# Optimization experiments

Measured on AMD Instinct MI355X. Metric: run time of the kernel, lower is better.

Reference implementation:

```python
import jax, jax.numpy as jnp
import numpy as np

N = 131072
K = 1024
D = 64

def setup_inputs() -> dict:
    key = jax.random.key(0)
    k1, k2 = jax.random.split(key)
    x = jax.random.normal(k1, (N, D), dtype=jnp.float32)
    emb_weight = jax.random.normal(k2, (K, D), dtype=jnp.float32)
    return {"x": x, "emb_weight": emb_weight}

def reference(x, emb_weight):
    distances = (
        jnp.sum(x * x, axis=1, keepdims=True)
        + jnp.sum(emb_weight * emb_weight, axis=1)
        - 2.0 * jnp.matmul(x, emb_weight.T)
    )
    codebook_indices = jnp.argmin(distances, axis=1)  # [N]
    probs = jax.nn.one_hot(codebook_indices, K, dtype=x.dtype)  # [N, K]
    z_q = emb_weight[codebook_indices]  # [N, D]
    return (z_q, probs)
```

## Files before the change

kernel.cpp:

```cpp
#include <hip/hip_runtime.h>
#include <math.h>

#define N_TOK 131072
#define K_CB  1024
#define D_DIM 64
#define MARGIN 0.0625f

#define WS_EN     0
#define WS_ES     4096
#define WS_CNT    266240
#define WS_LIST   266248

#define FILL_BLOCKS 2048
#define PREP_BLOCKS 16

typedef short bf16x8 __attribute__((ext_vector_type(8)));
typedef float f32x4  __attribute__((ext_vector_type(4)));

__device__ __forceinline__ ushort f2bf(float f) {
    uint u = __float_as_uint(f);
    u += 0x7FFFu + ((u >> 16) & 1u);
    return (ushort)(u >> 16);
}
__device__ __forceinline__ float bf2f(ushort h) {
    return __uint_as_float(((uint)h) << 16);
}

__global__ __launch_bounds__(256) void fill_and_prep(
    float* __restrict__ probs, const float* __restrict__ emb,
    float* __restrict__ en, ushort* __restrict__ es, uint* __restrict__ fixcnt)
{
    const int tid = threadIdx.x;
    const int blk = blockIdx.x;
    if (blk < FILL_BLOCKS) {
        f32x4* p = (f32x4*)probs + (size_t)blk * 16384 + tid;
        const f32x4 zero4 = {0.f, 0.f, 0.f, 0.f};
        #pragma unroll
        for (int i = 0; i < 64; ++i) p[i * 256] = zero4;
        return;
    }
    const int pb   = blk - FILL_BLOCKS;
    const int c6   = tid & 63;
    const int q    = tid >> 6;
    const int code = pb * 64 + c6;
    if (pb == 0 && tid == 0) *fixcnt = 0;

    const float* er = emb + (size_t)code * D_DIM;
    #pragma unroll
    for (int j = 0; j < 16; ++j) {
        float f = er[q * 16 + j];
        ushort h = f2bf(f);
        es[(size_t)code * 128 + q * 16 + j]      = h;
        es[(size_t)code * 128 + 64 + q * 16 + j] = f2bf(f - bf2f(h));
    }
    if (q == 0) {
        float s = 0.f;
        #pragma unroll
        for (int d = 0; d < D_DIM; ++d) s = fmaf(er[d], er[d], s);
        en[code] = s;
    }
}

__global__ __launch_bounds__(256) void vq_main(
    const float* __restrict__ x, const float* __restrict__ emb,
    const float* __restrict__ en, const ushort* __restrict__ es,
    float* __restrict__ zq, float* __restrict__ probs,
    uint* __restrict__ fixcnt, uint* __restrict__ fixlist, uint fixcap)
{
    const int tid  = threadIdx.x;
    const int wave = tid >> 6, lane = tid & 63;
    const int quad = lane >> 4, l15 = lane & 15;
    const int blockRow = blockIdx.x * 128;
    const int waveRow  = blockRow + wave * 32;

    __shared__ uint  lds_k[128];
    __shared__ float lds_en[K_CB];

    {
        f32x4 v = ((const f32x4*)en)[tid];
        ((f32x4*)lds_en)[tid] = v;
    }

    bf16x8 af[2][4];
    #pragma unroll
    for (int g = 0; g < 2; ++g) {
        const float* xr = x + (size_t)(waveRow + g * 16 + l15) * D_DIM + quad * 8;
        f32x4 p0 = *(const f32x4*)(xr);
        f32x4 p1 = *(const f32x4*)(xr + 4);
        f32x4 p2 = *(const f32x4*)(xr + 32);
        f32x4 p3 = *(const f32x4*)(xr + 36);
        float v0[8], v1[8];
        #pragma unroll
        for (int j = 0; j < 4; ++j) { v0[j] = p0[j]; v0[4 + j] = p1[j]; v1[j] = p2[j]; v1[4 + j] = p3[j]; }
        #pragma unroll
        for (int j = 0; j < 8; ++j) {
            ushort h0 = f2bf(v0[j]);
            af[g][0][j] = (short)h0;
            af[g][2][j] = (short)f2bf(v0[j] - bf2f(h0));
            ushort h1 = f2bf(v1[j]);
            af[g][1][j] = (short)h1;
            af[g][3][j] = (short)f2bf(v1[j] - bf2f(h1));
        }
    }
    __syncthreads();

    float b1[8], b2[8]; int k1[8];
    #pragma unroll
    for (int s = 0; s < 8; ++s) { b1[s] = INFINITY; b2[s] = INFINITY; k1[s] = 0; }

    const bf16x8* __restrict__ esv = (const bf16x8*)es;

    for (int cb = 0; cb < 64; ++cb) {
        const int code = cb * 16 + l15;
        bf16x8 bfr[4];
        #pragma unroll
        for (int ks = 0; ks < 4; ++ks) bfr[ks] = esv[(size_t)code * 16 + ks * 4 + quad];

        f32x4 acc0 = {0.f, 0.f, 0.f, 0.f};
        f32x4 acc1 = {0.f, 0.f, 0.f, 0.f};
        acc0 = __builtin_amdgcn_mfma_f32_16x16x32_bf16(af[0][0], bfr[0], acc0, 0, 0, 0);
        acc0 = __builtin_amdgcn_mfma_f32_16x16x32_bf16(af[0][1], bfr[1], acc0, 0, 0, 0);
        acc0 = __builtin_amdgcn_mfma_f32_16x16x32_bf16(af[0][0], bfr[2], acc0, 0, 0, 0);
        acc0 = __builtin_amdgcn_mfma_f32_16x16x32_bf16(af[0][1], bfr[3], acc0, 0, 0, 0);
        acc0 = __builtin_amdgcn_mfma_f32_16x16x32_bf16(af[0][2], bfr[0], acc0, 0, 0, 0);
        acc0 = __builtin_amdgcn_mfma_f32_16x16x32_bf16(af[0][3], bfr[1], acc0, 0, 0, 0);
        acc1 = __builtin_amdgcn_mfma_f32_16x16x32_bf16(af[1][0], bfr[0], acc1, 0, 0, 0);
        acc1 = __builtin_amdgcn_mfma_f32_16x16x32_bf16(af[1][1], bfr[1], acc1, 0, 0, 0);
        acc1 = __builtin_amdgcn_mfma_f32_16x16x32_bf16(af[1][0], bfr[2], acc1, 0, 0, 0);
        acc1 = __builtin_amdgcn_mfma_f32_16x16x32_bf16(af[1][1], bfr[3], acc1, 0, 0, 0);
        acc1 = __builtin_amdgcn_mfma_f32_16x16x32_bf16(af[1][2], bfr[0], acc1, 0, 0, 0);
        acc1 = __builtin_amdgcn_mfma_f32_16x16x32_bf16(af[1][3], bfr[1], acc1, 0, 0, 0);

        const float env = lds_en[code];
        #pragma unroll
        for (int r = 0; r < 4; ++r) {
            {
                float d = fmaf(-2.f, acc0[r], env);
                bool lt = d < b1[r];
                b2[r] = lt ? b1[r] : fminf(b2[r], d);
                k1[r] = lt ? code : k1[r];
                b1[r] = lt ? d : b1[r];
            }
            {
                int s = 4 + r;
                float d = fmaf(-2.f, acc1[r], env);
                bool lt = d < b1[s];
                b2[s] = lt ? b1[s] : fminf(b2[s], d);
                k1[s] = lt ? code : k1[s];
                b1[s] = lt ? d : b1[s];
            }
        }
    }

    #pragma unroll
    for (int s = 0; s < 8; ++s) {
        #pragma unroll
        for (int off = 1; off < 16; off <<= 1) {
            float ob1 = __shfl_xor(b1[s], off);
            int   ok1 = __shfl_xor(k1[s], off);
            float ob2 = __shfl_xor(b2[s], off);
            bool better = (ob1 < b1[s]) || (ob1 == b1[s] && ok1 < k1[s]);
            float loser = better ? b1[s] : ob1;
            b1[s] = better ? ob1 : b1[s];
            k1[s] = better ? ok1 : k1[s];
            b2[s] = fminf(fminf(b2[s], ob2), loser);
        }
    }
    if (l15 == 0) {
        #pragma unroll
        for (int s = 0; s < 8; ++s) {
            int g = s >> 2, r = s & 3;
            int lrow = wave * 32 + g * 16 + quad * 4 + r;
            uint word = (uint)k1[s];
            if (b2[s] - b1[s] <= MARGIN) word |= 0x80000000u;
            lds_k[lrow] = word;
        }
    }
    __syncthreads();

    if (tid < 128) {
        uint w = lds_k[tid];
        uint kk = w & 0x3FFu;
        probs[(size_t)(blockRow + tid) * K_CB + kk] = 1.0f;
        if (w & 0x80000000u) {
            uint idx = atomicAdd(fixcnt, 1u);
            if (idx < fixcap) fixlist[idx] = (uint)(blockRow + tid) | (kk << 17);
        }
    }

    #pragma unroll
    for (int t = 0; t < 8; ++t) {
        int i = tid + t * 256;
        int r = i >> 4, c = i & 15;
        int kk = (int)(lds_k[r] & 0x3FFu);
        f32x4 v = ((const f32x4*)(emb + (size_t)kk * D_DIM))[c];
        ((f32x4*)(zq + (size_t)(blockRow + r) * D_DIM))[c] = v;
    }
}

__global__ __launch_bounds__(256) void vq_fixup(
    const float* __restrict__ x, const float* __restrict__ emb,
    const float* __restrict__ en,
    float* __restrict__ zq, float* __restrict__ probs,
    const uint* __restrict__ fixcnt, const uint* __restrict__ fixlist, uint fixcap)
{
    const int lane = threadIdx.x & 63;
    const uint gwave = (uint)((blockIdx.x * 256 + threadIdx.x) >> 6);
    uint cnt = *fixcnt;
    if (cnt > fixcap) cnt = fixcap;

    for (uint e = gwave; e < cnt; e += 1024u) {
        uint w = fixlist[e];
        int row = (int)(w & 0x1FFFFu);
        int kg  = (int)(w >> 17);
        const float* xr = x + (size_t)row * D_DIM;
        float xn = 0.f;
        #pragma unroll
        for (int d = 0; d < D_DIM; ++d) xn = fmaf(xr[d], xr[d], xn);

        float bd = INFINITY; int bk = 0;
        for (int t = 0; t < 16; ++t) {
            int code = t * 64 + lane;
            const float* er = emb + (size_t)code * D_DIM;
            float a0 = 0.f, a1 = 0.f, a2 = 0.f, a3 = 0.f;
            #pragma unroll
            for (int d = 0; d < D_DIM; d += 4) {
                a0 = fmaf(xr[d + 0], er[d + 0], a0);
                a1 = fmaf(xr[d + 1], er[d + 1], a1);
                a2 = fmaf(xr[d + 2], er[d + 2], a2);
                a3 = fmaf(xr[d + 3], er[d + 3], a3);
            }
            float acc = (a0 + a1) + (a2 + a3);
            float dist = fmaf(-2.f, acc, xn + en[code]);
            if (dist < bd) { bd = dist; bk = code; }
        }
        #pragma unroll
        for (int off = 1; off < 64; off <<= 1) {
            float od = __shfl_xor(bd, off);
            int   ok = __shfl_xor(bk, off);
            if (od < bd || (od == bd && ok < bk)) { bd = od; bk = ok; }
        }
        if (bk != kg) {
            if (lane == 0) {
                probs[(size_t)row * K_CB + kg] = 0.f;
                probs[(size_t)row * K_CB + bk] = 1.f;
            }
            if (lane < 16)
                ((f32x4*)(zq + (size_t)row * D_DIM))[lane] =
                    ((const f32x4*)(emb + (size_t)bk * D_DIM))[lane];
        }
    }
}

extern "C" void kernel_launch(void* const* d_in, const int* in_sizes, int n_in,
                              void* d_out, int out_size, void* d_ws, size_t ws_size,
                              hipStream_t stream) {
    const float* x   = (const float*)d_in[0];
    const float* emb = (const float*)d_in[1];
    float* zq    = (float*)d_out;
    float* probs = (float*)d_out + (size_t)N_TOK * D_DIM;

    char* ws = (char*)d_ws;
    float*  en      = (float*)(ws + WS_EN);
    ushort* es      = (ushort*)(ws + WS_ES);
    uint*   fixcnt  = (uint*)(ws + WS_CNT);
    uint*   fixlist = (uint*)(ws + WS_LIST);
    uint fixcap = (ws_size > WS_LIST + 4) ? (uint)((ws_size - WS_LIST) / 4) : 0u;

    fill_and_prep<<<FILL_BLOCKS + PREP_BLOCKS, 256, 0, stream>>>(probs, emb, en, es, fixcnt);
    vq_main<<<N_TOK / 128, 256, 0, stream>>>(x, emb, en, es, zq, probs, fixcnt, fixlist, fixcap);
    vq_fixup<<<256, 256, 0, stream>>>(x, emb, en, zq, probs, fixcnt, fixlist, fixcap);
}
```

Before: 773.0 us.

## Fuse one-hot probs write into main kernel and halve rows per block

Removes the separate zero-fill pass over the 512MB probs tensor. The main kernel now writes each full one-hot row itself with nontemporal vector stores, so probs is written once instead of being zeroed and then scattered into. Each block now handles 64 rows, one 16-row MFMA group per wave. The LDS copy of the code norms and the block barriers are gone, and norms are read from global memory instead. The trade-off is that the matmul phase now carries the heavy store traffic inline, and each wave gets half the codebook reuse per load.

```diff
diff --git a/kernel.cpp b/kernel.cpp
--- a/kernel.cpp
+++ b/kernel.cpp
@@ -11,9 +11,6 @@
 #define WS_CNT    266240
 #define WS_LIST   266248
 
-#define FILL_BLOCKS 2048
-#define PREP_BLOCKS 16
-
 typedef short bf16x8 __attribute__((ext_vector_type(8)));
 typedef float f32x4  __attribute__((ext_vector_type(4)));
 
@@ -26,22 +23,14 @@
     return __uint_as_float(((uint)h) << 16);
 }
 
-__global__ __launch_bounds__(256) void fill_and_prep(
-    float* __restrict__ probs, const float* __restrict__ emb,
-    float* __restrict__ en, ushort* __restrict__ es, uint* __restrict__ fixcnt)
+__global__ __launch_bounds__(256) void prep_kernel(
+    const float* __restrict__ emb, float* __restrict__ en,
+    ushort* __restrict__ es, uint* __restrict__ fixcnt)
 {
     const int tid = threadIdx.x;
-    const int blk = blockIdx.x;
-    if (blk < FILL_BLOCKS) {
-        f32x4* p = (f32x4*)probs + (size_t)blk * 16384 + tid;
-        const f32x4 zero4 = {0.f, 0.f, 0.f, 0.f};
-        #pragma unroll
-        for (int i = 0; i < 64; ++i) p[i * 256] = zero4;
-        return;
-    }
-    const int pb   = blk - FILL_BLOCKS;
-    const int c6   = tid & 63;
-    const int q    = tid >> 6;
+    const int pb  = blockIdx.x;
+    const int c6  = tid & 63;
+    const int q   = tid >> 6;
     const int code = pb * 64 + c6;
     if (pb == 0 && tid == 0) *fixcnt = 0;
 
@@ -61,7 +50,7 @@
     }
 }
 
-__global__ __launch_bounds__(256) void vq_main(
+__global__ __launch_bounds__(256) void vq_onehot(
     const float* __restrict__ x, const float* __restrict__ emb,
     const float* __restrict__ en, const ushort* __restrict__ es,
     float* __restrict__ zq, float* __restrict__ probs,
@@ -70,21 +59,11 @@
     const int tid  = threadIdx.x;
     const int wave = tid >> 6, lane = tid & 63;
     const int quad = lane >> 4, l15 = lane & 15;
-    const int blockRow = blockIdx.x * 128;
-    const int waveRow  = blockRow + wave * 32;
-
-    __shared__ uint  lds_k[128];
-    __shared__ float lds_en[K_CB];
-
+    const int waveRow = blockIdx.x * 64 + wave * 16;
+
+    bf16x8 af[4];
     {
-        f32x4 v = ((const f32x4*)en)[tid];
-        ((f32x4*)lds_en)[tid] = v;
-    }
-
-    bf16x8 af[2][4];
-    #pragma unroll
-    for (int g = 0; g < 2; ++g) {
-        const float* xr = x + (size_t)(waveRow + g * 16 + l15) * D_DIM + quad * 8;
+        const float* xr = x + (size_t)(waveRow + l15) * D_DIM + quad * 8;
         f32x4 p0 = *(const f32x4*)(xr);
         f32x4 p1 = *(const f32x4*)(xr + 4);
         f32x4 p2 = *(const f32x4*)(xr + 32);
@@ -95,18 +74,17 @@
         #pragma unroll
         for (int j = 0; j < 8; ++j) {
             ushort h0 = f2bf(v0[j]);
-            af[g][0][j] = (short)h0;
-            af[g][2][j] = (short)f2bf(v0[j] - bf2f(h0));
+            af[0][j] = (short)h0;
+            af[2][j] = (short)f2bf(v0[j] - bf2f(h0));
             ushort h1 = f2bf(v1[j]);
-            af[g][1][j] = (short)h1;
-            af[g][3][j] = (short)f2bf(v1[j] - bf2f(h1));
-        }
-    }
-    __syncthreads();
-
-    float b1[8], b2[8]; int k1[8];
-    #pragma unroll
-    for (int s = 0; s < 8; ++s) { b1[s] = INFINITY; b2[s] = INFINITY; k1[s] = 0; }
+            af[1][j] = (short)h1;
+            af[3][j] = (short)f2bf(v1[j] - bf2f(h1));
+        }
+    }
+
+    float b1[4], b2[4]; int k1[4];
+    #pragma unroll
+    for (int r = 0; r < 4; ++r) { b1[r] = INFINITY; b2[r] = INFINITY; k1[r] = 0; }
 
     const bf16x8* __restrict__ esv = (const bf16x8*)es;
 
@@ -116,85 +94,66 @@
         #pragma unroll
         for (int ks = 0; ks < 4; ++ks) bfr[ks] = esv[(size_t)code * 16 + ks * 4 + quad];
 
-        f32x4 acc0 = {0.f, 0.f, 0.f, 0.f};
-        f32x4 acc1 = {0.f, 0.f, 0.f, 0.f};
-        acc0 = __builtin_amdgcn_mfma_f32_16x16x32_bf16(af[0][0], bfr[0], acc0, 0, 0, 0);
-        acc0 = __builtin_amdgcn_mfma_f32_16x16x32_bf16(af[0][1], bfr[1], acc0, 0, 0, 0);
-        acc0 = __builtin_amdgcn_mfma_f32_16x16x32_bf16(af[0][0], bfr[2], acc0, 0, 0, 0);
-        acc0 = __builtin_amdgcn_mfma_f32_16x16x32_bf16(af[0][1], bfr[3], acc0, 0, 0, 0);
-        acc0 = __builtin_amdgcn_mfma_f32_16x16x32_bf16(af[0][2], bfr[0], acc0, 0, 0, 0);
-        acc0 = __builtin_amdgcn_mfma_f32_16x16x32_bf16(af[0][3], bfr[1], acc0, 0, 0, 0);
-        acc1 = __builtin_amdgcn_mfma_f32_16x16x32_bf16(af[1][0], bfr[0], acc1, 0, 0, 0);
-        acc1 = __builtin_amdgcn_mfma_f32_16x16x32_bf16(af[1][1], bfr[1], acc1, 0, 0, 0);
-        acc1 = __builtin_amdgcn_mfma_f32_16x16x32_bf16(af[1][0], bfr[2], acc1, 0, 0, 0);
-        acc1 = __builtin_amdgcn_mfma_f32_16x16x32_bf16(af[1][1], bfr[3], acc1, 0, 0, 0);
-        acc1 = __builtin_amdgcn_mfma_f32_16x16x32_bf16(af[1][2], bfr[0], acc1, 0, 0, 0);
-        acc1 = __builtin_amdgcn_mfma_f32_16x16x32_bf16(af[1][3], bfr[1], acc1, 0, 0, 0);
-
-        const float env = lds_en[code];
+        f32x4 acc = {0.f, 0.f, 0.f, 0.f};
+        acc = __builtin_amdgcn_mfma_f32_16x16x32_bf16(af[0], bfr[0], acc, 0, 0, 0);
+        acc = __builtin_amdgcn_mfma_f32_16x16x32_bf16(af[1], bfr[1], acc, 0, 0, 0);
+        acc = __builtin_amdgcn_mfma_f32_16x16x32_bf16(af[0], bfr[2], acc, 0, 0, 0);
+        acc = __builtin_amdgcn_mfma_f32_16x16x32_bf16(af[1], bfr[3], acc, 0, 0, 0);
+        acc = __builtin_amdgcn_mfma_f32_16x16x32_bf16(af[2], bfr[0], acc, 0, 0, 0);
+        acc = __builtin_amdgcn_mfma_f32_16x16x32_bf16(af[3], bfr[1], acc, 0, 0, 0);
+
+        const float env = en[code];
         #pragma unroll
         for (int r = 0; r < 4; ++r) {
-            {
-                float d = fmaf(-2.f, acc0[r], env);
-                bool lt = d < b1[r];
-                b2[r] = lt ? b1[r] : fminf(b2[r], d);
-                k1[r] = lt ? code : k1[r];
-                b1[r] = lt ? d : b1[r];
-            }
-            {
-                int s = 4 + r;
-                float d = fmaf(-2.f, acc1[r], env);
-                bool lt = d < b1[s];
-                b2[s] = lt ? b1[s] : fminf(b2[s], d);
-                k1[s] = lt ? code : k1[s];
-                b1[s] = lt ? d : b1[s];
-            }
-        }
-    }
-
-    #pragma unroll
-    for (int s = 0; s < 8; ++s) {
+            float d = fmaf(-2.f, acc[r], env);
+            bool lt = d < b1[r];
+            b2[r] = lt ? b1[r] : fminf(b2[r], d);
+            k1[r] = lt ? code : k1[r];
+            b1[r] = lt ? d : b1[r];
+        }
+    }
+
+    #pragma unroll
+    for (int r = 0; r < 4; ++r) {
         #pragma unroll
         for (int off = 1; off < 16; off <<= 1) {
-            float ob1 = __shfl_xor(b1[s], off);
-            int   ok1 = __shfl_xor(k1[s], off);
-            float ob2 = __shfl_xor(b2[s], off);
-            bool better = (ob1 < b1[s]) || (ob1 == b1[s] && ok1 < k1[s]);
-            float loser = better ? b1[s] : ob1;
-            b1[s] = better ? ob1 : b1[s];
-            k1[s] = better ? ok1 : k1[s];
-            b2[s] = fminf(fminf(b2[s], ob2), loser);
-        }
-    }
-    if (l15 == 0) {
-        #pragma unroll
-        for (int s = 0; s < 8; ++s) {
-            int g = s >> 2, r = s & 3;
-            int lrow = wave * 32 + g * 16 + quad * 4 + r;
-            uint word = (uint)k1[s];
-            if (b2[s] - b1[s] <= MARGIN) word |= 0x80000000u;
-            lds_k[lrow] = word;
-        }
-    }
-    __syncthreads();
-
-    if (tid < 128) {
-        uint w = lds_k[tid];
-        uint kk = w & 0x3FFu;
-        probs[(size_t)(blockRow + tid) * K_CB + kk] = 1.0f;
-        if (w & 0x80000000u) {
+            float ob1 = __shfl_xor(b1[r], off);
+            int   ok1 = __shfl_xor(k1[r], off);
+            float ob2 = __shfl_xor(b2[r], off);
+            bool better = (ob1 < b1[r]) || (ob1 == b1[r] && ok1 < k1[r]);
+            float loser = better ? b1[r] : ob1;
+            b1[r] = better ? ob1 : b1[r];
+            k1[r] = better ? ok1 : k1[r];
+            b2[r] = fminf(fminf(b2[r], ob2), loser);
+        }
+    }
+
+    #pragma unroll
+    for (int m = 0; m < 16; ++m) {
+        const int src = (m >> 2) << 4;
+        const int   bk  = __shfl(k1[m & 3], src);
+        const float bb1 = __shfl(b1[m & 3], src);
+        const float bb2 = __shfl(b2[m & 3], src);
+        const int grow = waveRow + m;
+
+        float* prow = probs + (size_t)grow * K_CB;
+        #pragma unroll
+        for (int s = 0; s < 4; ++s) {
+            int c = s * 256 + lane * 4;
+            f32x4 v;
+            v[0] = (c     == bk) ? 1.f : 0.f;
+            v[1] = (c + 1 == bk) ? 1.f : 0.f;
+            v[2] = (c + 2 == bk) ? 1.f : 0.f;
+            v[3] = (c + 3 == bk) ? 1.f : 0.f;
+            __builtin_nontemporal_store(v, (f32x4*)(prow + c));
+        }
+        if (lane < 16)
+            ((f32x4*)(zq + (size_t)grow * D_DIM))[lane] =
+                ((const f32x4*)(emb + (size_t)bk * D_DIM))[lane];
+        if (lane == 0 && bb2 - bb1 <= MARGIN) {
             uint idx = atomicAdd(fixcnt, 1u);
-            if (idx < fixcap) fixlist[idx] = (uint)(blockRow + tid) | (kk << 17);
-        }
-    }
-
-    #pragma unroll
-    for (int t = 0; t < 8; ++t) {
-        int i = tid + t * 256;
-        int r = i >> 4, c = i & 15;
-        int kk = (int)(lds_k[r] & 0x3FFu);
-        f32x4 v = ((const f32x4*)(emb + (size_t)kk * D_DIM))[c];
-        ((f32x4*)(zq + (size_t)(blockRow + r) * D_DIM))[c] = v;
+            if (idx < fixcap) fixlist[idx] = (uint)grow | ((uint)bk << 17);
+        }
     }
 }
 
@@ -267,7 +226,7 @@
     uint*   fixlist = (uint*)(ws + WS_LIST);
     uint fixcap = (ws_size > WS_LIST + 4) ? (uint)((ws_size - WS_LIST) / 4) : 0u;
 
-    fill_and_prep<<<FILL_BLOCKS + PREP_BLOCKS, 256, 0, stream>>>(probs, emb, en, es, fixcnt);
-    vq_main<<<N_TOK / 128, 256, 0, stream>>>(x, emb, en, es, zq, probs, fixcnt, fixlist, fixcap);
+    prep_kernel<<<16, 256, 0, stream>>>(emb, en, es, fixcnt);
+    vq_onehot<<<N_TOK / 64, 256, 0, stream>>>(x, emb, en, es, zq, probs, fixcnt, fixlist, fixcap);
     vq_fixup<<<256, 256, 0, stream>>>(x, emb, en, zq, probs, fixcnt, fixlist, fixcap);
 }
```

Measured after the change: 826.1 us. 6.9% more time.
